# Kernel tuning notes

Hardware: AMD Instinct MI355X
Metric: run time of the kernel (lower is better)

## Reference

```python
import jax, jax.numpy as jnp
import numpy as np

N_NODES = 50000
N_EDGES = 1600000
KSIZE = 5   # kernel_size per dim
DIM = 3     # pseudo-coordinate dim


def spline_conv(x, src, dst, pseudo, W, root, bias, num_nodes):
    # Open B-spline basis, degree 1 (PyG SplineConv defaults).
    pos = pseudo * (KSIZE - 1)                         # [E, 3]
    idx = jnp.clip(jnp.floor(pos), 0, KSIZE - 2).astype(jnp.int32)
    frac = pos - idx                                   # [E, 3]
    strides = jnp.array([1, KSIZE, KSIZE * KSIZE], dtype=jnp.int32)
    x_j = x[src]                                       # [E, in]
    msg = jnp.zeros((src.shape[0], W.shape[-1]), x.dtype)
    # 2^dim = 8 active basis combinations per edge (small fixed loop).
    for b in range(2 ** DIM):
        bits = np.array([(b >> d) & 1 for d in range(DIM)])
        kidx = ((idx + jnp.asarray(bits, jnp.int32)) * strides).sum(-1)   # [E]
        basis = jnp.prod(jnp.where(jnp.asarray(bits, bool), frac, 1.0 - frac), axis=-1)  # [E]
        msg = msg + basis[:, None] * jnp.einsum('ei,eio->eo', x_j, W[kidx])
    out = jax.ops.segment_sum(msg, dst, num_segments=num_nodes)
    return out + x @ root + bias


def setup_inputs() -> dict:
    key = jax.random.key(0)
    ks = jax.random.split(key, 8)
    x = jax.random.normal(ks[0], (N_NODES, 1), jnp.float32)
    edge_index = jax.random.randint(ks[1], (2, N_EDGES), 0, N_NODES, jnp.int64)
    pseudo = jax.random.uniform(ks[2], (N_EDGES, DIM), jnp.float32)
    K = KSIZE ** DIM
    W1 = jax.random.normal(ks[3], (K, 1, 8), jnp.float32) * 0.1
    root1 = jax.random.normal(ks[4], (1, 8), jnp.float32) * 0.1
    bias1 = jnp.zeros((8,), jnp.float32)
    W2 = jax.random.normal(ks[5], (K, 8, 1), jnp.float32) * 0.1
    root2 = jax.random.normal(ks[6], (8, 1), jnp.float32) * 0.1
    bias2 = jnp.zeros((1,), jnp.float32)
    return {"x": x, "edge_index": edge_index, "pseudo": pseudo,
            "W1": W1, "root1": root1, "bias1": bias1,
            "W2": W2, "root2": root2, "bias2": bias2}


def reference(x, edge_index, pseudo, W1, root1, bias1, W2, root2, bias2):
    src = edge_index[0]
    dst = edge_index[1]
    n = x.shape[0]
    h = jax.nn.elu(spline_conv(x, src, dst, pseudo, W1, root1, bias1, n))
    out = jax.nn.elu(spline_conv(h, src, dst, pseudo, W2, root2, bias2, n))
    return out.reshape(-1)
```

## Files before the change

kernel.cpp:

```cpp
#include <hip/hip_runtime.h>
#include <math.h>

#define NK    125
#define HID   8
#define BSH   6
#define BKT   64
#define CAP   2560
#define MAXNB 1024
#define CHUNK 2816
#define WS    12

__device__ __forceinline__ float eluf(float v) {
    return v > 0.f ? v : expf(v) - 1.f;
}


__global__ __launch_bounds__(256) void init_cursor(int* __restrict__ cursor, int NB) {
    int b = blockIdx.x * 256 + threadIdx.x;
    if (b < NB) cursor[b] = b * CAP;
}

__global__ __launch_bounds__(256) void partition_edges(
    const int* __restrict__ src, const int* __restrict__ dst,
    const float* __restrict__ pseudo,
    int* __restrict__ cursor, int4* __restrict__ payload,
    int E, int NB)
{
    __shared__ int4 stage[CHUNK];
    __shared__ unsigned short perm[CHUNK];
    __shared__ unsigned short sb[CHUNK];
    __shared__ int s_off[MAXNB + 1];
    __shared__ int s_gmo[MAXNB];

    int e0  = blockIdx.x * CHUNK;
    int cnt = min(CHUNK, E - e0);

    for (int b = threadIdx.x; b < NB; b += 256) s_off[b] = 0;
    __syncthreads();

    for (int i = threadIdx.x; i < cnt; i += 256) {
        int e = e0 + i;
        int d = dst[e];
        float p0 = pseudo[3 * e + 0] * 4.f;
        float p1 = pseudo[3 * e + 1] * 4.f;
        float p2 = pseudo[3 * e + 2] * 4.f;
        int i0 = min(max((int)floorf(p0), 0), 3);
        int i1 = min(max((int)floorf(p1), 0), 3);
        int i2 = min(max((int)floorf(p2), 0), 3);
        float f0 = p0 - (float)i0, f1 = p1 - (float)i1, f2 = p2 - (float)i2;
        int kb = i0 + 5 * i1 + 25 * i2;
        int packed = src[e] | (kb << 16) | ((d & (BKT - 1)) << 23);
        stage[i] = make_int4(packed, __float_as_int(f0),
                             __float_as_int(f1), __float_as_int(f2));
        atomicAdd(&s_off[d >> BSH], 1);
    }
    __syncthreads();

    if (threadIdx.x < 64) {
        int per = (NB + 63) >> 6;
        int lo = threadIdx.x * per, hi = min(lo + per, NB);
        int sum = 0;
        for (int b = lo; b < hi; ++b) { int v = s_off[b]; s_off[b] = sum; sum += v; }
        int incl = sum;
        for (int d2 = 1; d2 < 64; d2 <<= 1) {
            int u = __shfl_up(incl, d2, 64);
            if ((int)threadIdx.x >= d2) incl += u;
        }
        int basep = incl - sum;
        for (int b = lo; b < hi; ++b) s_off[b] += basep;
        if (threadIdx.x == 63) s_off[NB] = incl;
    }
    __syncthreads();

    for (int b = threadIdx.x; b < NB; b += 256) {
        int c = s_off[b + 1] - s_off[b];
        int g = c ? atomicAdd(&cursor[b], c) : 0;
        s_gmo[b] = g - s_off[b];
    }
    __syncthreads();

    for (int i = threadIdx.x; i < cnt; i += 256) {
        int b = dst[e0 + i] >> BSH;
        int r = atomicAdd(&s_off[b], 1);
        perm[r] = (unsigned short)i;
        sb[r]   = (unsigned short)b;
    }
    __syncthreads();

    for (int o = threadIdx.x; o < cnt; o += 256) {
        int b = sb[o];
        int g = s_gmo[b] + o;
        if (g < (b + 1) * CAP)
            payload[g] = stage[perm[o]];
    }
}

__global__ __launch_bounds__(512) void layer1_fused(
    int4* __restrict__ payload, const int* __restrict__ cursor,
    const float* __restrict__ x, const float* __restrict__ W1,
    const float* __restrict__ root1, const float* __restrict__ bias1,
    float* __restrict__ h, int* __restrict__ ns, int* __restrict__ ne, int N)
{
    __shared__ float sW[NK * WS];
    __shared__ int4 stage[CAP];
    __shared__ unsigned short perm[CAP];
    __shared__ int hist[BKT];
    __shared__ int off[BKT + 1];
    __shared__ int cur[BKT];

    for (int i = threadIdx.x; i < NK * HID; i += 512)
        sW[(i >> 3) * WS + (i & 7)] = W1[i];
    if (threadIdx.x < BKT) hist[threadIdx.x] = 0;
    __syncthreads();

    int bkt  = blockIdx.x;
    int base = bkt * CAP;
    int cnt  = min(cursor[bkt] - base, CAP);

    for (int i = threadIdx.x; i < cnt; i += 512) {
        int4 pl = payload[base + i];
        stage[i] = pl;
        atomicAdd(&hist[(pl.x >> 23) & (BKT - 1)], 1);
    }
    __syncthreads();

    if (threadIdx.x < BKT) {
        int v = hist[threadIdx.x];
        int incl = v;
        for (int d = 1; d < BKT; d <<= 1) {
            int u = __shfl_up(incl, d, 64);
            if (threadIdx.x >= d) incl += u;
        }
        off[threadIdx.x + 1] = incl;
        if (threadIdx.x == 0) off[0] = 0;
        cur[threadIdx.x] = incl - v;
    }
    __syncthreads();

    for (int i = threadIdx.x; i < cnt; i += 512) {
        int nl = (stage[i].x >> 23) & (BKT - 1);
        int pos = atomicAdd(&cur[nl], 1);
        perm[pos] = (unsigned short)i;
    }
    __syncthreads();

    for (int i = threadIdx.x; i < cnt; i += 512)
        payload[base + i] = stage[perm[i]];
    if (threadIdx.x < BKT) {
        int n = (bkt << BSH) + threadIdx.x;
        if (n < N) {
            ns[n] = base + off[threadIdx.x];
            ne[n] = base + off[threadIdx.x + 1];
        }
    }

    int nl = threadIdx.x >> 3;
    int j  = threadIdx.x & 7;
    int s = off[nl], e = off[nl + 1];

    float4 aclo = make_float4(0.f, 0.f, 0.f, 0.f);
    float4 achi = make_float4(0.f, 0.f, 0.f, 0.f);

    for (int i = s + j; i < e; i += 8) {
        int4 pl = stage[perm[i]];
        int packed = pl.x;
        float f0 = __int_as_float(pl.y);
        float f1 = __int_as_float(pl.z);
        float f2 = __int_as_float(pl.w);
        int sidx = packed & 0xFFFF;
        int kb   = (packed >> 16) & 0x7F;
        float xj = x[sidx];
#pragma unroll
        for (int b = 0; b < 8; ++b) {
            int kidx = kb + (b & 1) + ((b >> 1) & 1) * 5 + ((b >> 2) & 1) * 25;
            float basis = ((b & 1) ? f0 : 1.f - f0)
                        * ((b & 2) ? f1 : 1.f - f1)
                        * ((b & 4) ? f2 : 1.f - f2);
            float w = xj * basis;
            float4 wlo = *(const float4*)&sW[kidx * WS];
            float4 whi = *(const float4*)&sW[kidx * WS + 4];
            aclo.x += w * wlo.x; aclo.y += w * wlo.y;
            aclo.z += w * wlo.z; aclo.w += w * wlo.w;
            achi.x += w * whi.x; achi.y += w * whi.y;
            achi.z += w * whi.z; achi.w += w * whi.w;
        }
    }

    float acc[HID] = {aclo.x, aclo.y, aclo.z, aclo.w, achi.x, achi.y, achi.z, achi.w};
#pragma unroll
    for (int m = 1; m < 8; m <<= 1)
#pragma unroll
        for (int o = 0; o < HID; ++o)
            acc[o] += __shfl_xor(acc[o], m, 64);

    int n = (bkt << BSH) + nl;
    if (n < N) {
        float v = acc[j] + x[n] * root1[j] + bias1[j];
        h[(size_t)n * HID + j] = eluf(v);
    }
}

__global__ __launch_bounds__(256) void layer2_csr(
    const int4* __restrict__ payload, const int* __restrict__ ns,
    const int* __restrict__ ne, const float* __restrict__ h,
    const float* __restrict__ W2, const float* __restrict__ root2,
    const float* __restrict__ bias2, float* __restrict__ out, int N)
{
    __shared__ float sW[NK * WS];
    for (int i = threadIdx.x; i < NK * HID; i += 256)
        sW[(i >> 3) * WS + (i & 7)] = W2[i];
    __syncthreads();

    int n = blockIdx.x * 32 + (threadIdx.x >> 3);
    int j = threadIdx.x & 7;
    int s = 0, e = 0;
    if (n < N) { s = ns[n]; e = ne[n]; }

    float msg = 0.f;
    for (int i = s + j; i < e; i += 8) {
        int4 pl = payload[i];
        int packed = pl.x;
        float f0 = __int_as_float(pl.y);
        float f1 = __int_as_float(pl.z);
        float f2 = __int_as_float(pl.w);
        int sidx = packed & 0xFFFF;
        int kb   = (packed >> 16) & 0x7F;
        const float4* hp = (const float4*)(h + (size_t)sidx * HID);
        float4 ha = hp[0];
        float4 hb = hp[1];
#pragma unroll
        for (int b = 0; b < 8; ++b) {
            int kidx = kb + (b & 1) + ((b >> 1) & 1) * 5 + ((b >> 2) & 1) * 25;
            float basis = ((b & 1) ? f0 : 1.f - f0)
                        * ((b & 2) ? f1 : 1.f - f1)
                        * ((b & 4) ? f2 : 1.f - f2);
            float4 wlo = *(const float4*)&sW[kidx * WS];
            float4 whi = *(const float4*)&sW[kidx * WS + 4];
            float dot = ha.x * wlo.x + ha.y * wlo.y + ha.z * wlo.z + ha.w * wlo.w
                      + hb.x * whi.x + hb.y * whi.y + hb.z * whi.z + hb.w * whi.w;
            msg += basis * dot;
        }
    }

    if (n < N) msg += h[(size_t)n * HID + j] * root2[j];

#pragma unroll
    for (int m = 1; m < 8; m <<= 1)
        msg += __shfl_xor(msg, m, 64);

    if (j == 0 && n < N)
        out[n] = eluf(msg + bias2[0]);
}


__global__ __launch_bounds__(256) void spline_edge1(
    const int* __restrict__ src, const int* __restrict__ dst,
    const float* __restrict__ pseudo, const float* __restrict__ x,
    const float* __restrict__ W1, float* __restrict__ hacc, int E)
{
    __shared__ float sW[HID * NK];
    for (int i = threadIdx.x; i < HID * NK; i += blockDim.x) {
        int k = i >> 3, o = i & 7;
        sW[o * NK + k] = W1[i];
    }
    __syncthreads();
    int e = blockIdx.x * blockDim.x + threadIdx.x;
    if (e >= E) return;
    float p0 = pseudo[3 * e + 0] * 4.f, p1 = pseudo[3 * e + 1] * 4.f, p2 = pseudo[3 * e + 2] * 4.f;
    int i0 = min(max((int)floorf(p0), 0), 3);
    int i1 = min(max((int)floorf(p1), 0), 3);
    int i2 = min(max((int)floorf(p2), 0), 3);
    float f0 = p0 - i0, f1 = p1 - i1, f2 = p2 - i2;
    int kbase = i0 + 5 * i1 + 25 * i2;
    float xj = x[src[e]];
    float acc[HID];
#pragma unroll
    for (int o = 0; o < HID; ++o) acc[o] = 0.f;
#pragma unroll
    for (int b = 0; b < 8; ++b) {
        int kidx = kbase + (b & 1) + ((b >> 1) & 1) * 5 + ((b >> 2) & 1) * 25;
        float basis = ((b & 1) ? f0 : 1.f - f0) * ((b & 2) ? f1 : 1.f - f1) * ((b & 4) ? f2 : 1.f - f2);
#pragma unroll
        for (int o = 0; o < HID; ++o) acc[o] += basis * sW[o * NK + kidx];
    }
    float* hp = hacc + (size_t)dst[e] * HID;
#pragma unroll
    for (int o = 0; o < HID; ++o) atomicAdd(hp + o, xj * acc[o]);
}

__global__ __launch_bounds__(256) void node1(
    float* __restrict__ h, const float* __restrict__ x,
    const float* __restrict__ root1, const float* __restrict__ bias1, int N)
{
    int t = blockIdx.x * blockDim.x + threadIdx.x;
    if (t >= N * HID) return;
    int n = t >> 3, o = t & 7;
    h[t] = eluf(h[t] + x[n] * root1[o] + bias1[o]);
}

__global__ __launch_bounds__(256) void spline_edge2(
    const int* __restrict__ src, const int* __restrict__ dst,
    const float* __restrict__ pseudo, const float* __restrict__ h,
    const float* __restrict__ W2, float* __restrict__ oacc, int E)
{
    __shared__ float sW[HID * NK];
    for (int idx = threadIdx.x; idx < HID * NK; idx += blockDim.x) {
        int k = idx >> 3, i = idx & 7;
        sW[i * NK + k] = W2[idx];
    }
    __syncthreads();
    int e = blockIdx.x * blockDim.x + threadIdx.x;
    if (e >= E) return;
    float p0 = pseudo[3 * e + 0] * 4.f, p1 = pseudo[3 * e + 1] * 4.f, p2 = pseudo[3 * e + 2] * 4.f;
    int i0 = min(max((int)floorf(p0), 0), 3);
    int i1 = min(max((int)floorf(p1), 0), 3);
    int i2 = min(max((int)floorf(p2), 0), 3);
    float f0 = p0 - i0, f1 = p1 - i1, f2 = p2 - i2;
    int kbase = i0 + 5 * i1 + 25 * i2;
    const float4* hp4 = (const float4*)(h + (size_t)src[e] * HID);
    float4 ha = hp4[0], hb = hp4[1];
    float hj[HID] = {ha.x, ha.y, ha.z, ha.w, hb.x, hb.y, hb.z, hb.w};
    float msg = 0.f;
#pragma unroll
    for (int b = 0; b < 8; ++b) {
        int kidx = kbase + (b & 1) + ((b >> 1) & 1) * 5 + ((b >> 2) & 1) * 25;
        float basis = ((b & 1) ? f0 : 1.f - f0) * ((b & 2) ? f1 : 1.f - f1) * ((b & 4) ? f2 : 1.f - f2);
        float dot = 0.f;
#pragma unroll
        for (int i = 0; i < HID; ++i) dot += hj[i] * sW[i * NK + kidx];
        msg += basis * dot;
    }
    atomicAdd(&oacc[dst[e]], msg);
}

__global__ __launch_bounds__(256) void node2(
    const float* __restrict__ oacc, const float* __restrict__ h,
    const float* __restrict__ root2, const float* __restrict__ bias2,
    float* __restrict__ out, int N)
{
    int n = blockIdx.x * blockDim.x + threadIdx.x;
    if (n >= N) return;
    float v = oacc[n] + bias2[0];
#pragma unroll
    for (int i = 0; i < HID; ++i) v += h[(size_t)n * HID + i] * root2[i];
    out[n] = eluf(v);
}


extern "C" void kernel_launch(void* const* d_in, const int* in_sizes, int n_in,
                              void* d_out, int out_size, void* d_ws, size_t ws_size,
                              hipStream_t stream) {
    const float* x      = (const float*)d_in[0];
    const int*   ei     = (const int*)d_in[1];
    const float* pseudo = (const float*)d_in[2];
    const float* W1     = (const float*)d_in[3];
    const float* root1  = (const float*)d_in[4];
    const float* bias1  = (const float*)d_in[5];
    const float* W2     = (const float*)d_in[6];
    const float* root2  = (const float*)d_in[7];
    const float* bias2  = (const float*)d_in[8];

    int N = in_sizes[0];
    int E = in_sizes[1] / 2;
    const int* src = ei;
    const int* dst = ei + E;

    int NB = (N + BKT - 1) >> BSH;
    size_t payload_bytes = (size_t)NB * CAP * sizeof(int4);
    size_t h_bytes       = (size_t)N * HID * sizeof(float);
    size_t cursor_bytes  = (size_t)NB * sizeof(int);
    size_t nsne_bytes    = (size_t)N * sizeof(int);
    size_t need = payload_bytes + h_bytes + cursor_bytes + 2 * nsne_bytes + 64;

    if (NB <= MAXNB && N <= 65536 && ws_size >= need) {
        char* p = (char*)d_ws;
        int4*  payload = (int4*)p;                 p += payload_bytes;
        float* h       = (float*)p;                p += h_bytes;
        int*   cursor  = (int*)p;                  p += cursor_bytes;
        int*   ns      = (int*)p;                  p += nsne_bytes;
        int*   ne      = (int*)p;

        init_cursor<<<(NB + 255) / 256, 256, 0, stream>>>(cursor, NB);
        int pblocks = (E + CHUNK - 1) / CHUNK;
        partition_edges<<<pblocks, 256, 0, stream>>>(src, dst, pseudo, cursor, payload, E, NB);
        layer1_fused<<<NB, 512, 0, stream>>>(payload, cursor, x, W1, root1, bias1, h, ns, ne, N);
        layer2_csr<<<(N + 31) / 32, 256, 0, stream>>>(payload, ns, ne, h, W2, root2, bias2, (float*)d_out, N);
    } else {
        float* h    = (float*)d_ws;
        float* oacc = h + (size_t)N * HID;
        hipMemsetAsync(d_ws, 0, (size_t)(N * HID + N) * sizeof(float), stream);
        int eg = (E + 255) / 256;
        spline_edge1<<<eg, 256, 0, stream>>>(src, dst, pseudo, x, W1, h, E);
        node1<<<(N * HID + 255) / 256, 256, 0, stream>>>(h, x, root1, bias1, N);
        spline_edge2<<<eg, 256, 0, stream>>>(src, dst, pseudo, h, W2, oacc, E);
        node2<<<(N + 255) / 256, 256, 0, stream>>>(oacc, h, root2, bias2, (float*)d_out, N);
    }
}
```

Measured before the change: 167.9 us.

## Switch per-node lanes from edge-split to output-channel split; cache bucket ids in partition

In both aggregation kernels, each of the 8 lanes per node now owns one hidden channel and loops over every edge of the node, where before the edges were strided across lanes. This removes the 8-wide shuffle reduction and the float4 weight loads, and layer 2 loads one h element per lane instead of two float4. The cost is that every lane redundantly reads each edge payload and recomputes the basis, and the serial edge loop per node grows 8x. The partition kernel also caches the bucket id in shared memory instead of re-reading dst, and CHUNK shrinks from 2816 to 2048.

```diff
diff --git a/kernel.cpp b/kernel.cpp
--- a/kernel.cpp
+++ b/kernel.cpp
@@ -7,7 +7,7 @@
 #define BKT   64
 #define CAP   2560
 #define MAXNB 1024
-#define CHUNK 2816
+#define CHUNK 2048
 #define WS    12
 
 __device__ __forceinline__ float eluf(float v) {
@@ -52,7 +52,9 @@
         int packed = src[e] | (kb << 16) | ((d & (BKT - 1)) << 23);
         stage[i] = make_int4(packed, __float_as_int(f0),
                              __float_as_int(f1), __float_as_int(f2));
-        atomicAdd(&s_off[d >> BSH], 1);
+        int b = d >> BSH;
+        sb[i] = (unsigned short)b;
+        atomicAdd(&s_off[b], 1);
     }
     __syncthreads();
 
@@ -80,18 +82,17 @@
     __syncthreads();
 
     for (int i = threadIdx.x; i < cnt; i += 256) {
-        int b = dst[e0 + i] >> BSH;
-        int r = atomicAdd(&s_off[b], 1);
+        int r = atomicAdd(&s_off[sb[i]], 1);
         perm[r] = (unsigned short)i;
-        sb[r]   = (unsigned short)b;
     }
     __syncthreads();
 
     for (int o = threadIdx.x; o < cnt; o += 256) {
-        int b = sb[o];
+        int i = perm[o];
+        int b = sb[i];
         int g = s_gmo[b] + o;
         if (g < (b + 1) * CAP)
-            payload[g] = stage[perm[o]];
+            payload[g] = stage[i];
     }
 }
 
@@ -158,10 +159,8 @@
     int j  = threadIdx.x & 7;
     int s = off[nl], e = off[nl + 1];
 
-    float4 aclo = make_float4(0.f, 0.f, 0.f, 0.f);
-    float4 achi = make_float4(0.f, 0.f, 0.f, 0.f);
-
-    for (int i = s + j; i < e; i += 8) {
+    float acc = 0.f;
+    for (int i = s; i < e; ++i) {
         int4 pl = stage[perm[i]];
         int packed = pl.x;
         float f0 = __int_as_float(pl.y);
@@ -176,26 +175,13 @@
             float basis = ((b & 1) ? f0 : 1.f - f0)
                         * ((b & 2) ? f1 : 1.f - f1)
                         * ((b & 4) ? f2 : 1.f - f2);
-            float w = xj * basis;
-            float4 wlo = *(const float4*)&sW[kidx * WS];
-            float4 whi = *(const float4*)&sW[kidx * WS + 4];
-            aclo.x += w * wlo.x; aclo.y += w * wlo.y;
-            aclo.z += w * wlo.z; aclo.w += w * wlo.w;
-            achi.x += w * whi.x; achi.y += w * whi.y;
-            achi.z += w * whi.z; achi.w += w * whi.w;
-        }
-    }
-
-    float acc[HID] = {aclo.x, aclo.y, aclo.z, aclo.w, achi.x, achi.y, achi.z, achi.w};
-#pragma unroll
-    for (int m = 1; m < 8; m <<= 1)
-#pragma unroll
-        for (int o = 0; o < HID; ++o)
-            acc[o] += __shfl_xor(acc[o], m, 64);
+            acc += (xj * basis) * sW[kidx * WS + j];
+        }
+    }
 
     int n = (bkt << BSH) + nl;
     if (n < N) {
-        float v = acc[j] + x[n] * root1[j] + bias1[j];
+        float v = acc + x[n] * root1[j] + bias1[j];
         h[(size_t)n * HID + j] = eluf(v);
     }
 }
@@ -217,7 +203,7 @@
     if (n < N) { s = ns[n]; e = ne[n]; }
 
     float msg = 0.f;
-    for (int i = s + j; i < e; i += 8) {
+    for (int i = s; i < e; ++i) {
         int4 pl = payload[i];
         int packed = pl.x;
         float f0 = __int_as_float(pl.y);
@@ -225,21 +211,17 @@
         float f2 = __int_as_float(pl.w);
         int sidx = packed & 0xFFFF;
         int kb   = (packed >> 16) & 0x7F;
-        const float4* hp = (const float4*)(h + (size_t)sidx * HID);
-        float4 ha = hp[0];
-        float4 hb = hp[1];
+        float hj = h[(size_t)sidx * HID + j];
+        float wsum = 0.f;
 #pragma unroll
         for (int b = 0; b < 8; ++b) {
             int kidx = kb + (b & 1) + ((b >> 1) & 1) * 5 + ((b >> 2) & 1) * 25;
             float basis = ((b & 1) ? f0 : 1.f - f0)
                         * ((b & 2) ? f1 : 1.f - f1)
                         * ((b & 4) ? f2 : 1.f - f2);
-            float4 wlo = *(const float4*)&sW[kidx * WS];
-            float4 whi = *(const float4*)&sW[kidx * WS + 4];
-            float dot = ha.x * wlo.x + ha.y * wlo.y + ha.z * wlo.z + ha.w * wlo.w
-                      + hb.x * whi.x + hb.y * whi.y + hb.z * whi.z + hb.w * whi.w;
-            msg += basis * dot;
-        }
+            wsum += basis * sW[kidx * WS + j];
+        }
+        msg += hj * wsum;
     }
 
     if (n < N) msg += h[(size_t)n * HID + j] * root2[j];
```

Result: slower. 194.0 us (+15.6%).

## Shrink partition staging to int2 and defer pseudo basis math to scatter

Applied to the files above, without the earlier changes.

The partition kernel now stages only a packed src/local-node/bucket word plus the edge id (int2) in shared memory, instead of the full int4 payload. The pseudo-coordinate loads and basis-index computation move into the final scatter loop, and the separate bucket-id array is dropped because the bucket is recovered from the packed word. Halving the staging footprint lets the chunk grow to 5120 edges with 512 threads per block, meaning fewer blocks and fewer global cursor atomics. The cost is that pseudo is now read in permuted, less coalesced order, and the fast path gains a guard requiring E < 2^24.

```diff
diff --git a/kernel.cpp b/kernel.cpp
--- a/kernel.cpp
+++ b/kernel.cpp
@@ -7,7 +7,8 @@
 #define BKT   64
 #define CAP   2560
 #define MAXNB 1024
-#define CHUNK 2816
+#define CHUNK 5120
+#define PTHR  512
 #define WS    12
 
 __device__ __forceinline__ float eluf(float v) {
@@ -20,39 +21,29 @@
     if (b < NB) cursor[b] = b * CAP;
 }
 
-__global__ __launch_bounds__(256) void partition_edges(
+__global__ __launch_bounds__(PTHR) void partition_edges(
     const int* __restrict__ src, const int* __restrict__ dst,
     const float* __restrict__ pseudo,
     int* __restrict__ cursor, int4* __restrict__ payload,
     int E, int NB)
 {
-    __shared__ int4 stage[CHUNK];
+    __shared__ int2 stage[CHUNK];
     __shared__ unsigned short perm[CHUNK];
-    __shared__ unsigned short sb[CHUNK];
     __shared__ int s_off[MAXNB + 1];
     __shared__ int s_gmo[MAXNB];
 
     int e0  = blockIdx.x * CHUNK;
     int cnt = min(CHUNK, E - e0);
 
-    for (int b = threadIdx.x; b < NB; b += 256) s_off[b] = 0;
-    __syncthreads();
-
-    for (int i = threadIdx.x; i < cnt; i += 256) {
+    for (int b = threadIdx.x; b < NB; b += PTHR) s_off[b] = 0;
+    __syncthreads();
+
+    for (int i = threadIdx.x; i < cnt; i += PTHR) {
         int e = e0 + i;
         int d = dst[e];
-        float p0 = pseudo[3 * e + 0] * 4.f;
-        float p1 = pseudo[3 * e + 1] * 4.f;
-        float p2 = pseudo[3 * e + 2] * 4.f;
-        int i0 = min(max((int)floorf(p0), 0), 3);
-        int i1 = min(max((int)floorf(p1), 0), 3);
-        int i2 = min(max((int)floorf(p2), 0), 3);
-        float f0 = p0 - (float)i0, f1 = p1 - (float)i1, f2 = p2 - (float)i2;
-        int kb = i0 + 5 * i1 + 25 * i2;
-        int packed = src[e] | (kb << 16) | ((d & (BKT - 1)) << 23);
-        stage[i] = make_int4(packed, __float_as_int(f0),
-                             __float_as_int(f1), __float_as_int(f2));
-        atomicAdd(&s_off[d >> BSH], 1);
+        int b = d >> BSH;
+        stage[i] = make_int2(src[e] | ((d & (BKT - 1)) << 16) | (b << 22), e);
+        atomicAdd(&s_off[b], 1);
     }
     __syncthreads();
 
@@ -72,26 +63,40 @@
     }
     __syncthreads();
 
-    for (int b = threadIdx.x; b < NB; b += 256) {
+    for (int b = threadIdx.x; b < NB; b += PTHR) {
         int c = s_off[b + 1] - s_off[b];
         int g = c ? atomicAdd(&cursor[b], c) : 0;
         s_gmo[b] = g - s_off[b];
     }
     __syncthreads();
 
-    for (int i = threadIdx.x; i < cnt; i += 256) {
-        int b = dst[e0 + i] >> BSH;
-        int r = atomicAdd(&s_off[b], 1);
+    for (int i = threadIdx.x; i < cnt; i += PTHR) {
+        unsigned ux = (unsigned)stage[i].x;
+        int r = atomicAdd(&s_off[ux >> 22], 1);
         perm[r] = (unsigned short)i;
-        sb[r]   = (unsigned short)b;
-    }
-    __syncthreads();
-
-    for (int o = threadIdx.x; o < cnt; o += 256) {
-        int b = sb[o];
+    }
+    __syncthreads();
+
+    for (int o = threadIdx.x; o < cnt; o += PTHR) {
+        int i = perm[o];
+        unsigned ux = (unsigned)stage[i].x;
+        int e  = stage[i].y;
+        int sidx = ux & 0xFFFF;
+        int nl   = (ux >> 16) & (BKT - 1);
+        int b    = ux >> 22;
+        float p0 = pseudo[3 * e + 0] * 4.f;
+        float p1 = pseudo[3 * e + 1] * 4.f;
+        float p2 = pseudo[3 * e + 2] * 4.f;
+        int i0 = min(max((int)floorf(p0), 0), 3);
+        int i1 = min(max((int)floorf(p1), 0), 3);
+        int i2 = min(max((int)floorf(p2), 0), 3);
+        float f0 = p0 - (float)i0, f1 = p1 - (float)i1, f2 = p2 - (float)i2;
+        int kb = i0 + 5 * i1 + 25 * i2;
         int g = s_gmo[b] + o;
         if (g < (b + 1) * CAP)
-            payload[g] = stage[perm[o]];
+            payload[g] = make_int4(sidx | (kb << 16) | (nl << 23),
+                                   __float_as_int(f0), __float_as_int(f1),
+                                   __float_as_int(f2));
     }
 }
 
@@ -372,7 +377,7 @@
     size_t nsne_bytes    = (size_t)N * sizeof(int);
     size_t need = payload_bytes + h_bytes + cursor_bytes + 2 * nsne_bytes + 64;
 
-    if (NB <= MAXNB && N <= 65536 && ws_size >= need) {
+    if (NB <= MAXNB && N <= 65536 && E < (1 << 24) && ws_size >= need) {
         char* p = (char*)d_ws;
         int4*  payload = (int4*)p;                 p += payload_bytes;
         float* h       = (float*)p;                p += h_bytes;
@@ -382,7 +387,7 @@
 
         init_cursor<<<(NB + 255) / 256, 256, 0, stream>>>(cursor, NB);
         int pblocks = (E + CHUNK - 1) / CHUNK;
-        partition_edges<<<pblocks, 256, 0, stream>>>(src, dst, pseudo, cursor, payload, E, NB);
+        partition_edges<<<pblocks, PTHR, 0, stream>>>(src, dst, pseudo, cursor, payload, E, NB);
         layer1_fused<<<NB, 512, 0, stream>>>(payload, cursor, x, W1, root1, bias1, h, ns, ne, N);
         layer2_csr<<<(N + 31) / 32, 256, 0, stream>>>(payload, ns, ne, h, W2, root2, bias2, (float*)d_out, N);
     } else {
```

Result: no change. 165.0 us (-1.7%).
